# Optimization experiments

Hardware: AMD Instinct MI355X
Metric: run time of the kernel (lower is better)

## Reference

```python
import jax, jax.numpy as jnp
import numpy as np

P_DROP = 0.6  # F.dropout default training=True in the original forward

def setup_inputs() -> dict:
    key = jax.random.key(0)
    k1, k2, k3, k4 = jax.random.split(key, 4)
    B, T, V, F, K, O = 32, 12, 1000, 64, 3, 64
    x = jax.random.normal(k1, (B, T, V, F), dtype=jnp.float32)
    Att = jax.random.uniform(k2, (V, V), dtype=jnp.float32)
    cheb = jax.random.normal(k3, (K, V, V), dtype=jnp.float32)   # Chebyshev polynomials T_k(L)
    Theta = jax.random.normal(k4, (K, F, O), dtype=jnp.float32)  # per-order feature transforms
    return {"x": x, "Att": Att, "cheb": cheb, "Theta": Theta}

def reference(x, Att, cheb, Theta):
    # x: [B,T,V,F]; Att: [V,V]; cheb: [K,V,V]; Theta: [K,F,O]
    B, T, V, F = x.shape
    K = cheb.shape[0]
    keep = 1.0 - P_DROP
    # Original draws a fresh dropout mask per (time_step, k); replicate with a fixed key.
    mask = jax.random.bernoulli(jax.random.key(42), keep, (T, K, V, V))
    TkA = cheb * Att                                   # [K,V,V] attention-weighted polynomial
    M = jnp.where(mask, TkA[None] / keep, 0.0)         # [T,K,V,V] inverted dropout
    # rhs = T_k_with_at @ graph_signal, batched over (b,t,k)
    rhs = jnp.einsum('tkuv,btvf->btkuf', M, x)         # [B,T,K,V,F]
    # sum_k rhs_k @ Theta_k  -> [B,T,V,O]; matches permute(0,3,1,2) of stacked outputs
    out = jnp.einsum('btkuf,kfo->btuo', rhs, Theta)
    return jax.nn.relu(out)
```

## Files before the change

kernel.cpp:

```cpp
#include <hip/hip_runtime.h>
#include <hip/hip_bf16.h>
#include <stdint.h>


typedef __attribute__((ext_vector_type(8))) short short8;
typedef __attribute__((ext_vector_type(4))) float f32x4;

__device__ __forceinline__ ushort f2bf(float f) {
  __hip_bfloat16 h = __float2bfloat16(f);
  return *reinterpret_cast<ushort*>(&h);
}

__device__ __forceinline__ void threefry2x32(uint32_t c0, uint32_t c1,
                                             uint32_t& o0, uint32_t& o1) {
  const uint32_t ks0 = 0u;
  const uint32_t ks1 = 42u;
  const uint32_t ks2 = ks0 ^ ks1 ^ 0x1BD11BDAu;
  uint32_t x0 = c0 + ks0;
  uint32_t x1 = c1 + ks1;
#define TFR(r) { x0 += x1; x1 = (x1 << (r)) | (x1 >> (32 - (r))); x1 ^= x0; }
  TFR(13) TFR(15) TFR(26) TFR(6)
  x0 += ks1; x1 += ks2 + 1u;
  TFR(17) TFR(29) TFR(16) TFR(24)
  x0 += ks2; x1 += ks0 + 2u;
  TFR(13) TFR(15) TFR(26) TFR(6)
  x0 += ks0; x1 += ks1 + 3u;
  TFR(17) TFR(29) TFR(16) TFR(24)
  x0 += ks1; x1 += ks2 + 4u;
  TFR(13) TFR(15) TFR(26) TFR(6)
  x0 += ks2; x1 += ks0 + 5u;
#undef TFR
  o0 = x0; o1 = x1;
}

__global__ void build_m(const float* __restrict__ Att,
                        const float* __restrict__ cheb,
                        ushort* __restrict__ Mf) {
  const uint32_t idx = blockIdx.x * 256u + threadIdx.x;
  const uint32_t j = idx & 7u;
  const uint32_t lane = (idx >> 3) & 63u;
  const uint32_t ks = (idx >> 9) & 1u;
  const uint32_t c = (idx >> 10) & 15u;
  const uint32_t u16 = (idx >> 14) & 63u;
  const uint32_t tk = idx >> 20;
  const uint32_t up = u16 * 16u + (lane & 15u);
  const uint32_t vp = c * 64u + ks * 32u + (lane >> 4) * 8u + j;
  float val = 0.f;
  if ((vp < 1000u) & (up < 1000u)) {
    const uint32_t flat = (tk * 1000u + up) * 1000u + vp;
    uint32_t o0, o1;
    threefry2x32(0u, flat, o0, o1);
    const uint32_t bits = o0 ^ o1;
    const float u = __uint_as_float((bits >> 9) | 0x3f800000u) - 1.0f;
    if (u < 0.4f) {
      val = cheb[(tk % 3u) * 1000000u + up * 1000u + vp] *
            Att[up * 1000u + vp] * 2.5f;
    }
  }
  Mf[idx] = f2bf(val);
}

__global__ void transpose_x(const float* __restrict__ x,
                            ushort* __restrict__ xt) {
  __shared__ float lt[64][65];
  const int vc = blockIdx.x, t = blockIdx.y, b = blockIdx.z;
  const int tid = threadIdx.x;
  const int v0 = vc * 64;
#pragma unroll
  for (int i = 0; i < 4; ++i) {
    const int c = i * 256 + tid;
    const int vi = c >> 4, f4 = c & 15;
    float4 q = make_float4(0.f, 0.f, 0.f, 0.f);
    if (v0 + vi < 1000)
      q = *(const float4*)(x + ((((size_t)b * 12 + t) * 1000 + v0 + vi) << 6) + f4 * 4);
    lt[f4 * 4 + 0][vi] = q.x;
    lt[f4 * 4 + 1][vi] = q.y;
    lt[f4 * 4 + 2][vi] = q.z;
    lt[f4 * 4 + 3][vi] = q.w;
  }
  __syncthreads();
  const int f = tid >> 2, g = tid & 3;
  alignas(16) ushort tmp[16];
#pragma unroll
  for (int j = 0; j < 16; ++j) tmp[j] = f2bf(lt[f][g * 16 + j]);
  const size_t base = ((size_t)(t * 2048 + b * 64 + f)) << 10;
  *(uint4*)(xt + base + v0 + g * 16)     = *(const uint4*)&tmp[0];
  *(uint4*)(xt + base + v0 + g * 16 + 8) = *(const uint4*)&tmp[8];
}

#define LDT 72

#define MFMA(a, b, c) __builtin_amdgcn_mfma_f32_16x16x32_bf16((a), (b), (c), 0, 0, 0)

#define BURST(BP)                                                             \
  do {                                                                        \
    const ushort* sBc = (BP);                                                 \
    _Pragma("unroll")                                                         \
    for (int ks = 0; ks < 2; ++ks) {                                          \
      short8 bv[4];                                                           \
      _Pragma("unroll")                                                       \
      for (int ni = 0; ni < 4; ++ni) {                                        \
        const int row = wn * 64 + ni * 16 + l15;                              \
        bv[ni] = *(const short8*)&sBc[row * 64 + (((ks * 4 + quad) ^ rsw) * 8)]; \
      }                                                                       \
      _Pragma("unroll")                                                       \
      for (int k = 0; k < 3; ++k)                                             \
        _Pragma("unroll")                                                     \
        for (int mi = 0; mi < 2; ++mi)                                        \
          _Pragma("unroll")                                                   \
          for (int ni = 0; ni < 4; ++ni)                                      \
            pacc[k][mi][ni] = MFMA(afr[k][mi][ks], bv[ni], pacc[k][mi][ni]);  \
    }                                                                         \
  } while (0)

#define LOAD_A(VC)                                                            \
  do {                                                                        \
    _Pragma("unroll")                                                         \
    for (int k = 0; k < 3; ++k)                                               \
      _Pragma("unroll")                                                       \
      for (int mi = 0; mi < 2; ++mi)                                          \
        _Pragma("unroll")                                                     \
        for (int ks = 0; ks < 2; ++ks)                                        \
          afr[k][mi][ks] = *(const short8*)(Mf + fb[k][mi] +                  \
                             (size_t)(VC) * 1024 + ks * 512 + lane * 8);      \
  } while (0)

#define SOFT_BARRIER()                                                        \
  do {                                                                        \
    asm volatile("s_waitcnt lgkmcnt(0)" ::: "memory");                        \
    __builtin_amdgcn_s_barrier();                                             \
    __builtin_amdgcn_sched_barrier(0);                                        \
  } while (0)

__global__ __launch_bounds__(512, 1)
void cheb_main(const ushort* __restrict__ Mf, const ushort* __restrict__ xt,
               const float* __restrict__ Theta, float* __restrict__ out) {
  __shared__ __align__(16) ushort smem[23040];
  const int tid = threadIdx.x;
  const int lane = tid & 63;
  const int w = tid >> 6;
  const int wu = w >> 1, wn = w & 1;
  const int quad = lane >> 4, l15 = lane & 15;
  const int bid = blockIdx.x;
  const int nt = (bid >> 3) & 15;
  const int ut = bid & 7;
  const int t  = bid >> 7;
  const int u0 = ut * 128, n0 = nt * 128;

  ushort* buf0 = smem;
  ushort* buf1 = smem + 8192;
  ushort* sP  = smem + w * (32 * LDT);
  ushort* sTh = smem + 18432;

  const int srow = lane >> 3;
  const int gchunk = (lane & 7) ^ srow;
  const int rsw = l15 & 7;

  const size_t xrow0 = (size_t)(t * 2048 + n0);
  const int rr0 = 8 * (w * 2 + 0) + srow;
  const int rr1 = 8 * (w * 2 + 1) + srow;
  const size_t gx0 = ((xrow0 + rr0) << 10) + gchunk * 8;
  const size_t gx1 = ((xrow0 + rr1) << 10) + gchunk * 8;
  const int da0 = (w * 2 + 0) * 512 + lane * 8;
  const int da1 = (w * 2 + 1) * 512 + lane * 8;

  size_t fb[3][2];
#pragma unroll
  for (int k = 0; k < 3; ++k)
#pragma unroll
    for (int mi = 0; mi < 2; ++mi)
      fb[k][mi] = ((size_t)((t * 3 + k) * 64 + ut * 8 + wu * 2 + mi)) << 14;

  f32x4 pacc[3][2][4];
#pragma unroll
  for (int k = 0; k < 3; ++k)
#pragma unroll
    for (int i = 0; i < 2; ++i)
#pragma unroll
      for (int j = 0; j < 4; ++j) pacc[k][i][j] = f32x4{0.f, 0.f, 0.f, 0.f};

  short8 afr[3][2][2];
  uint4 p0, p1;

  p0 = *(const uint4*)(xt + gx0);
  p1 = *(const uint4*)(xt + gx1);
  *(uint4*)&buf0[da0] = p0;
  *(uint4*)&buf0[da1] = p1;
  __syncthreads();

#pragma unroll 1
  for (int it = 0; it < 8; ++it) {
    const int vc = it * 2;
    LOAD_A(vc);
    p0 = *(const uint4*)(xt + gx0 + (size_t)(vc + 1) * 64);
    p1 = *(const uint4*)(xt + gx1 + (size_t)(vc + 1) * 64);
    __builtin_amdgcn_s_setprio(1);
    BURST(buf0);
    __builtin_amdgcn_s_setprio(0);
    *(uint4*)&buf1[da0] = p0;
    *(uint4*)&buf1[da1] = p1;
    SOFT_BARRIER();
    LOAD_A(vc + 1);
    if (vc + 1 < 15) {
      p0 = *(const uint4*)(xt + gx0 + (size_t)(vc + 2) * 64);
      p1 = *(const uint4*)(xt + gx1 + (size_t)(vc + 2) * 64);
    }
    __builtin_amdgcn_s_setprio(1);
    BURST(buf1);
    __builtin_amdgcn_s_setprio(0);
    if (vc + 1 < 15) {
      *(uint4*)&buf0[da0] = p0;
      *(uint4*)&buf0[da1] = p1;
    }
    SOFT_BARRIER();
  }

  f32x4 oacc[2][4];
#pragma unroll
  for (int i = 0; i < 2; ++i)
#pragma unroll
    for (int j = 0; j < 4; ++j) oacc[i][j] = f32x4{0.f, 0.f, 0.f, 0.f};

#pragma unroll
  for (int k = 0; k < 3; ++k) {
    __syncthreads();
#pragma unroll
    for (int mi = 0; mi < 2; ++mi)
#pragma unroll
      for (int ni = 0; ni < 4; ++ni)
#pragma unroll
        for (int r = 0; r < 4; ++r)
          sP[(mi * 16 + quad * 4 + r) * LDT + ni * 16 + l15] = f2bf(pacc[k][mi][ni][r]);
    for (int e = tid; e < 4096; e += 512) {
      const int f = e >> 6, o = e & 63;
      sTh[o * LDT + f] = f2bf(Theta[k * 4096 + e]);
    }
    __syncthreads();
#pragma unroll
    for (int ks = 0; ks < 2; ++ks) {
      short8 a2[2], b2[4];
#pragma unroll
      for (int mi = 0; mi < 2; ++mi)
        a2[mi] = *(const short8*)&sP[(mi * 16 + l15) * LDT + ks * 32 + quad * 8];
#pragma unroll
      for (int ni = 0; ni < 4; ++ni)
        b2[ni] = *(const short8*)&sTh[(ni * 16 + l15) * LDT + ks * 32 + quad * 8];
#pragma unroll
      for (int mi = 0; mi < 2; ++mi)
#pragma unroll
        for (int ni = 0; ni < 4; ++ni)
          oacc[mi][ni] = MFMA(a2[mi], b2[ni], oacc[mi][ni]);
    }
  }

#pragma unroll
  for (int mi = 0; mi < 2; ++mi) {
    const int u_base = u0 + wu * 32 + mi * 16 + quad * 4;
#pragma unroll
    for (int ni = 0; ni < 4; ++ni) {
      const int n = n0 + wn * 64 + ni * 16 + l15;
      const int b = n >> 6, oo = n & 63;
      float* op = out + (((size_t)b * 12 + t) * 1000) * 64 + oo;
#pragma unroll
      for (int r = 0; r < 4; ++r) {
        const int u = u_base + r;
        if (u < 1000) op[(size_t)u * 64] = fmaxf(oacc[mi][ni][r], 0.f);
      }
    }
  }
}

extern "C" void kernel_launch(void* const* d_in, const int* in_sizes, int n_in,
                              void* d_out, int out_size, void* d_ws, size_t ws_size,
                              hipStream_t stream) {
  const float* x     = (const float*)d_in[0];
  const float* Att   = (const float*)d_in[1];
  const float* cheb  = (const float*)d_in[2];
  const float* Theta = (const float*)d_in[3];
  float* out = (float*)d_out;

  ushort* Mf  = (ushort*)d_ws;
  ushort* xtw = Mf + 37748736ull;

  build_m<<<147456, 256, 0, stream>>>(Att, cheb, Mf);
  transpose_x<<<dim3(16, 12, 32), 256, 0, stream>>>(x, xtw);
  cheb_main<<<1536, 512, 0, stream>>>(Mf, xtw, Theta, out);
}
```

Before: 306.1 us.

## Reassociate Theta projection before graph GEMM and fuse K into reduction

```diff
diff --git a/kernel.cpp b/kernel.cpp
--- a/kernel.cpp
+++ b/kernel.cpp
@@ -9,6 +9,15 @@
 __device__ __forceinline__ ushort f2bf(float f) {
   __hip_bfloat16 h = __float2bfloat16(f);
   return *reinterpret_cast<ushort*>(&h);
+}
+
+__device__ __forceinline__ short8 cvt8(float4 a, float4 b) {
+  short8 r;
+  r[0] = (short)f2bf(a.x); r[1] = (short)f2bf(a.y);
+  r[2] = (short)f2bf(a.z); r[3] = (short)f2bf(a.w);
+  r[4] = (short)f2bf(b.x); r[5] = (short)f2bf(b.y);
+  r[6] = (short)f2bf(b.z); r[7] = (short)f2bf(b.w);
+  return r;
 }
 
 __device__ __forceinline__ void threefry2x32(uint32_t c0, uint32_t c1,
@@ -60,214 +69,199 @@
   Mf[idx] = f2bf(val);
 }
 
-__global__ void transpose_x(const float* __restrict__ x,
-                            ushort* __restrict__ xt) {
-  __shared__ float lt[64][65];
-  const int vc = blockIdx.x, t = blockIdx.y, b = blockIdx.z;
-  const int tid = threadIdx.x;
+#define MFMA(a, b, c) __builtin_amdgcn_mfma_f32_16x16x32_bf16((a), (b), (c), 0, 0, 0)
+
+__global__ __launch_bounds__(192, 1)
+void build_yt(const float* __restrict__ x, const float* __restrict__ Theta,
+              ushort* __restrict__ yt, int NR, int bq0) {
+  __shared__ __align__(16) ushort sm[13824];
+  const int tid = threadIdx.x, lane = tid & 63, w = tid >> 6;
+  const int quad = lane >> 4, l15 = lane & 15;
+  const int vc = blockIdx.x, t = blockIdx.y, bb = blockIdx.z;
+  const int b = bq0 + bb;
   const int v0 = vc * 64;
-#pragma unroll
-  for (int i = 0; i < 4; ++i) {
-    const int c = i * 256 + tid;
-    const int vi = c >> 4, f4 = c & 15;
-    float4 q = make_float4(0.f, 0.f, 0.f, 0.f);
-    if (v0 + vi < 1000)
-      q = *(const float4*)(x + ((((size_t)b * 12 + t) * 1000 + v0 + vi) << 6) + f4 * 4);
-    lt[f4 * 4 + 0][vi] = q.x;
-    lt[f4 * 4 + 1][vi] = q.y;
-    lt[f4 * 4 + 2][vi] = q.z;
-    lt[f4 * 4 + 3][vi] = q.w;
+
+  for (int e = tid; e < 12288; e += 192) {
+    const int k = e >> 12, rem = e & 4095, f = rem >> 6, o = rem & 63;
+    sm[k * 4608 + o * 72 + f] = f2bf(Theta[e]);
   }
   __syncthreads();
-  const int f = tid >> 2, g = tid & 3;
-  alignas(16) ushort tmp[16];
-#pragma unroll
-  for (int j = 0; j < 16; ++j) tmp[j] = f2bf(lt[f][g * 16 + j]);
-  const size_t base = ((size_t)(t * 2048 + b * 64 + f)) << 10;
-  *(uint4*)(xt + base + v0 + g * 16)     = *(const uint4*)&tmp[0];
-  *(uint4*)(xt + base + v0 + g * 16 + 8) = *(const uint4*)&tmp[8];
-}
-
-#define LDT 72
-
-#define MFMA(a, b, c) __builtin_amdgcn_mfma_f32_16x16x32_bf16((a), (b), (c), 0, 0, 0)
-
-#define BURST(BP)                                                             \
-  do {                                                                        \
-    const ushort* sBc = (BP);                                                 \
+
+  f32x4 pacc[4][4];
+#pragma unroll
+  for (int i = 0; i < 4; ++i)
+#pragma unroll
+    for (int j = 0; j < 4; ++j) pacc[i][j] = f32x4{0.f, 0.f, 0.f, 0.f};
+
+  const ushort* sTh = sm + w * 4608;
+  const float* xb = x + (((size_t)b * 12 + t) * 1000) * 64;
+
+#pragma unroll
+  for (int ks = 0; ks < 2; ++ks) {
+    short8 av[4], bv[4];
+#pragma unroll
+    for (int mi = 0; mi < 4; ++mi)
+      av[mi] = *(const short8*)&sTh[(mi * 16 + l15) * 72 + ks * 32 + quad * 8];
+#pragma unroll
+    for (int ni = 0; ni < 4; ++ni) {
+      const int v = v0 + ni * 16 + l15;
+      float4 c0 = make_float4(0.f, 0.f, 0.f, 0.f);
+      float4 c1 = make_float4(0.f, 0.f, 0.f, 0.f);
+      if (v < 1000) {
+        const float* row = xb + (size_t)v * 64 + ks * 32 + quad * 8;
+        c0 = *(const float4*)row;
+        c1 = *(const float4*)(row + 4);
+      }
+      bv[ni] = cvt8(c0, c1);
+    }
+#pragma unroll
+    for (int mi = 0; mi < 4; ++mi)
+#pragma unroll
+      for (int ni = 0; ni < 4; ++ni)
+        pacc[mi][ni] = MFMA(av[mi], bv[ni], pacc[mi][ni]);
+  }
+
+  ushort* sY = sm + w * 4608;
+#pragma unroll
+  for (int mi = 0; mi < 4; ++mi)
+#pragma unroll
+    for (int ni = 0; ni < 4; ++ni)
+#pragma unroll
+      for (int r = 0; r < 4; ++r)
+        sY[(mi * 16 + quad * 4 + r) * 72 + ni * 16 + l15] = f2bf(pacc[mi][ni][r]);
+
+  const int seg = lane & 7;
+#pragma unroll
+  for (int p = 0; p < 8; ++p) {
+    const int o = p * 8 + (lane >> 3);
+    const uint4 val = *(const uint4*)&sY[o * 72 + seg * 8];
+    *(uint4*)(yt + (((size_t)(w * 12 + t) * (size_t)NR + (size_t)bb * 64 + o) << 10)
+                 + v0 + seg * 8) = val;
+  }
+}
+
+#define LOAD_A(AR, C)                                                         \
+  do {                                                                        \
+    const size_t base_ = ((tk3 + (size_t)((C) >> 4)) << 20) +                 \
+                         ((size_t)((C) & 15) << 10) + lane * 8;               \
+    _Pragma("unroll")                                                         \
+    for (int mi = 0; mi < 4; ++mi)                                            \
+      _Pragma("unroll")                                                       \
+      for (int ks = 0; ks < 2; ++ks)                                          \
+        AR[mi][ks] = *(const short8*)(Mf + base_ +                            \
+                       ((size_t)(u16b + mi) << 14) + (ks << 9));              \
+  } while (0)
+
+#define LOAD_B(P0, P1, P2, P3, C)                                             \
+  do {                                                                        \
+    const size_t yb_ = (((size_t)(((C) >> 4) * 12 + t) * (size_t)NR + n0 +    \
+                         brow) << 10) + ((size_t)((C) & 15) << 6) + gch * 8;  \
+    P0 = *(const uint4*)(yt + yb_);                                           \
+    P1 = *(const uint4*)(yt + yb_ + (64 << 10));                              \
+    P2 = *(const uint4*)(yt + yb_ + (128 << 10));                             \
+    P3 = *(const uint4*)(yt + yb_ + (192 << 10));                             \
+  } while (0)
+
+#define WRITE_B(P0, P1, P2, P3, BUF)                                          \
+  do {                                                                        \
+    *(uint4*)&(BUF)[tid * 8]          = P0;                                   \
+    *(uint4*)&(BUF)[4096 + tid * 8]   = P1;                                   \
+    *(uint4*)&(BUF)[8192 + tid * 8]   = P2;                                   \
+    *(uint4*)&(BUF)[12288 + tid * 8]  = P3;                                   \
+  } while (0)
+
+#define BURST(BUF, AR)                                                        \
+  do {                                                                        \
     _Pragma("unroll")                                                         \
     for (int ks = 0; ks < 2; ++ks) {                                          \
       short8 bv[4];                                                           \
       _Pragma("unroll")                                                       \
       for (int ni = 0; ni < 4; ++ni) {                                        \
-        const int row = wn * 64 + ni * 16 + l15;                              \
-        bv[ni] = *(const short8*)&sBc[row * 64 + (((ks * 4 + quad) ^ rsw) * 8)]; \
+        const int row_ = wc * 64 + ni * 16 + l15;                             \
+        bv[ni] = *(const short8*)&(BUF)[row_ * 64 +                           \
+                                        ((((ks * 4 + quad) ^ rsw)) << 3)];    \
       }                                                                       \
       _Pragma("unroll")                                                       \
-      for (int k = 0; k < 3; ++k)                                             \
+      for (int mi = 0; mi < 4; ++mi)                                          \
         _Pragma("unroll")                                                     \
-        for (int mi = 0; mi < 2; ++mi)                                        \
-          _Pragma("unroll")                                                   \
-          for (int ni = 0; ni < 4; ++ni)                                      \
-            pacc[k][mi][ni] = MFMA(afr[k][mi][ks], bv[ni], pacc[k][mi][ni]);  \
+        for (int ni = 0; ni < 4; ++ni)                                        \
+          pacc[mi][ni] = MFMA(AR[mi][ks], bv[ni], pacc[mi][ni]);              \
     }                                                                         \
   } while (0)
 
-#define LOAD_A(VC)                                                            \
-  do {                                                                        \
-    _Pragma("unroll")                                                         \
-    for (int k = 0; k < 3; ++k)                                               \
-      _Pragma("unroll")                                                       \
-      for (int mi = 0; mi < 2; ++mi)                                          \
-        _Pragma("unroll")                                                     \
-        for (int ks = 0; ks < 2; ++ks)                                        \
-          afr[k][mi][ks] = *(const short8*)(Mf + fb[k][mi] +                  \
-                             (size_t)(VC) * 1024 + ks * 512 + lane * 8);      \
-  } while (0)
-
-#define SOFT_BARRIER()                                                        \
-  do {                                                                        \
-    asm volatile("s_waitcnt lgkmcnt(0)" ::: "memory");                        \
-    __builtin_amdgcn_s_barrier();                                             \
-    __builtin_amdgcn_sched_barrier(0);                                        \
-  } while (0)
-
-__global__ __launch_bounds__(512, 1)
-void cheb_main(const ushort* __restrict__ Mf, const ushort* __restrict__ xt,
-               const float* __restrict__ Theta, float* __restrict__ out) {
-  __shared__ __align__(16) ushort smem[23040];
-  const int tid = threadIdx.x;
-  const int lane = tid & 63;
-  const int w = tid >> 6;
-  const int wu = w >> 1, wn = w & 1;
-  const int quad = lane >> 4, l15 = lane & 15;
-  const int bid = blockIdx.x;
-  const int nt = (bid >> 3) & 15;
-  const int ut = bid & 7;
-  const int t  = bid >> 7;
-  const int u0 = ut * 128, n0 = nt * 128;
+__global__ __launch_bounds__(512, 2)
+void gemm_main(const ushort* __restrict__ Mf, const ushort* __restrict__ yt,
+               float* __restrict__ out, int NR, int bq0, int nblocks) {
+  __shared__ __align__(16) ushort smem[32768];
+  const int tid = threadIdx.x, lane = tid & 63, w = tid >> 6;
+  const int wr = w >> 2, wc = w & 3;
+  const int quad = lane >> 4, l15 = lane & 15, rsw = l15 & 7;
+  const int q = nblocks >> 3;
+  const int swz = ((int)blockIdx.x & 7) * q + ((int)blockIdx.x >> 3);
+  const int ntcnt = NR >> 8;
+  const int ntile = swz % ntcnt;
+  const int rem = swz / ntcnt;
+  const int ut = rem & 7, t = rem >> 3;
+  const int u0 = ut * 128, n0 = ntile * 256;
 
   ushort* buf0 = smem;
-  ushort* buf1 = smem + 8192;
-  ushort* sP  = smem + w * (32 * LDT);
-  ushort* sTh = smem + 18432;
-
-  const int srow = lane >> 3;
-  const int gchunk = (lane & 7) ^ srow;
-  const int rsw = l15 & 7;
-
-  const size_t xrow0 = (size_t)(t * 2048 + n0);
-  const int rr0 = 8 * (w * 2 + 0) + srow;
-  const int rr1 = 8 * (w * 2 + 1) + srow;
-  const size_t gx0 = ((xrow0 + rr0) << 10) + gchunk * 8;
-  const size_t gx1 = ((xrow0 + rr1) << 10) + gchunk * 8;
-  const int da0 = (w * 2 + 0) * 512 + lane * 8;
-  const int da1 = (w * 2 + 1) * 512 + lane * 8;
-
-  size_t fb[3][2];
-#pragma unroll
-  for (int k = 0; k < 3; ++k)
-#pragma unroll
-    for (int mi = 0; mi < 2; ++mi)
-      fb[k][mi] = ((size_t)((t * 3 + k) * 64 + ut * 8 + wu * 2 + mi)) << 14;
-
-  f32x4 pacc[3][2][4];
-#pragma unroll
-  for (int k = 0; k < 3; ++k)
-#pragma unroll
-    for (int i = 0; i < 2; ++i)
-#pragma unroll
-      for (int j = 0; j < 4; ++j) pacc[k][i][j] = f32x4{0.f, 0.f, 0.f, 0.f};
-
-  short8 afr[3][2][2];
-  uint4 p0, p1;
-
-  p0 = *(const uint4*)(xt + gx0);
-  p1 = *(const uint4*)(xt + gx1);
-  *(uint4*)&buf0[da0] = p0;
-  *(uint4*)&buf0[da1] = p1;
+  ushort* buf1 = smem + 16384;
+
+  const int gch = (tid & 7) ^ ((tid >> 3) & 7);
+  const int brow = tid >> 3;
+  const int u16b = ut * 8 + wr * 4;
+  const size_t tk3 = (size_t)(t * 3);
+
+  f32x4 pacc[4][4];
+#pragma unroll
+  for (int i = 0; i < 4; ++i)
+#pragma unroll
+    for (int j = 0; j < 4; ++j) pacc[i][j] = f32x4{0.f, 0.f, 0.f, 0.f};
+
+  short8 aA[4][2], aB[4][2];
+  uint4 p0, p1, p2, p3, q0, q1, q2, q3;
+
+  LOAD_B(p0, p1, p2, p3, 0);
+  WRITE_B(p0, p1, p2, p3, buf0);
+  LOAD_A(aA, 0);
   __syncthreads();
 
 #pragma unroll 1
-  for (int it = 0; it < 8; ++it) {
-    const int vc = it * 2;
-    LOAD_A(vc);
-    p0 = *(const uint4*)(xt + gx0 + (size_t)(vc + 1) * 64);
-    p1 = *(const uint4*)(xt + gx1 + (size_t)(vc + 1) * 64);
+  for (int it = 0; it < 24; ++it) {
+    const int c1 = it * 2 + 1;
+    LOAD_A(aB, it * 2 + 1);
+    LOAD_B(q0, q1, q2, q3, it * 2 + 1);
     __builtin_amdgcn_s_setprio(1);
-    BURST(buf0);
+    BURST(buf0, aA);
     __builtin_amdgcn_s_setprio(0);
-    *(uint4*)&buf1[da0] = p0;
-    *(uint4*)&buf1[da1] = p1;
-    SOFT_BARRIER();
-    LOAD_A(vc + 1);
-    if (vc + 1 < 15) {
-      p0 = *(const uint4*)(xt + gx0 + (size_t)(vc + 2) * 64);
-      p1 = *(const uint4*)(xt + gx1 + (size_t)(vc + 2) * 64);
+    WRITE_B(q0, q1, q2, q3, buf1);
+    __syncthreads();
+    if (c1 < 47) {
+      LOAD_A(aA, c1 + 1);
+      LOAD_B(p0, p1, p2, p3, c1 + 1);
     }
     __builtin_amdgcn_s_setprio(1);
-    BURST(buf1);
+    BURST(buf1, aB);
     __builtin_amdgcn_s_setprio(0);
-    if (vc + 1 < 15) {
-      *(uint4*)&buf0[da0] = p0;
-      *(uint4*)&buf0[da1] = p1;
-    }
-    SOFT_BARRIER();
-  }
-
-  f32x4 oacc[2][4];
-#pragma unroll
-  for (int i = 0; i < 2; ++i)
-#pragma unroll
-    for (int j = 0; j < 4; ++j) oacc[i][j] = f32x4{0.f, 0.f, 0.f, 0.f};
-
-#pragma unroll
-  for (int k = 0; k < 3; ++k) {
+    if (c1 < 47) WRITE_B(p0, p1, p2, p3, buf0);
     __syncthreads();
-#pragma unroll
-    for (int mi = 0; mi < 2; ++mi)
-#pragma unroll
-      for (int ni = 0; ni < 4; ++ni)
-#pragma unroll
-        for (int r = 0; r < 4; ++r)
-          sP[(mi * 16 + quad * 4 + r) * LDT + ni * 16 + l15] = f2bf(pacc[k][mi][ni][r]);
-    for (int e = tid; e < 4096; e += 512) {
-      const int f = e >> 6, o = e & 63;
-      sTh[o * LDT + f] = f2bf(Theta[k * 4096 + e]);
-    }
-    __syncthreads();
-#pragma unroll
-    for (int ks = 0; ks < 2; ++ks) {
-      short8 a2[2], b2[4];
-#pragma unroll
-      for (int mi = 0; mi < 2; ++mi)
-        a2[mi] = *(const short8*)&sP[(mi * 16 + l15) * LDT + ks * 32 + quad * 8];
-#pragma unroll
-      for (int ni = 0; ni < 4; ++ni)
-        b2[ni] = *(const short8*)&sTh[(ni * 16 + l15) * LDT + ks * 32 + quad * 8];
-#pragma unroll
-      for (int mi = 0; mi < 2; ++mi)
-#pragma unroll
-        for (int ni = 0; ni < 4; ++ni)
-          oacc[mi][ni] = MFMA(a2[mi], b2[ni], oacc[mi][ni]);
-    }
-  }
-
-#pragma unroll
-  for (int mi = 0; mi < 2; ++mi) {
-    const int u_base = u0 + wu * 32 + mi * 16 + quad * 4;
+  }
+
+  const int ubase = u0 + wr * 64;
+  const int nbase = n0 + wc * 64;
+#pragma unroll
+  for (int mi = 0; mi < 4; ++mi)
 #pragma unroll
     for (int ni = 0; ni < 4; ++ni) {
-      const int n = n0 + wn * 64 + ni * 16 + l15;
-      const int b = n >> 6, oo = n & 63;
-      float* op = out + (((size_t)b * 12 + t) * 1000) * 64 + oo;
+      const int n = nbase + ni * 16 + l15;
+      const int b = bq0 + (n >> 6), o = n & 63;
+      float* op = out + (((size_t)b * 12 + t) * 1000) * 64 + o;
 #pragma unroll
       for (int r = 0; r < 4; ++r) {
-        const int u = u_base + r;
-        if (u < 1000) op[(size_t)u * 64] = fmaxf(oacc[mi][ni][r], 0.f);
+        const int u = ubase + mi * 16 + quad * 4 + r;
+        if (u < 1000) op[(size_t)u * 64] = fmaxf(pacc[mi][ni][r], 0.f);
       }
     }
-  }
 }
 
 extern "C" void kernel_launch(void* const* d_in, const int* in_sizes, int n_in,
@@ -279,10 +273,18 @@
   const float* Theta = (const float*)d_in[3];
   float* out = (float*)d_out;
 
-  ushort* Mf  = (ushort*)d_ws;
-  ushort* xtw = Mf + 37748736ull;
+  ushort* Mf = (ushort*)d_ws;
+  ushort* yt = Mf + 37748736ull;
 
   build_m<<<147456, 256, 0, stream>>>(Att, cheb, Mf);
-  transpose_x<<<dim3(16, 12, 32), 256, 0, stream>>>(x, xtw);
-  cheb_main<<<1536, 512, 0, stream>>>(Mf, xtw, Theta, out);
-}
+
+  if (ws_size >= 226492416ull) {
+    build_yt<<<dim3(16, 12, 32), 192, 0, stream>>>(x, Theta, yt, 2048, 0);
+    gemm_main<<<768, 512, 0, stream>>>(Mf, yt, out, 2048, 0, 768);
+  } else {
+    for (int qq = 0; qq < 4; ++qq) {
+      build_yt<<<dim3(16, 12, 8), 192, 0, stream>>>(x, Theta, yt, 512, qq * 8);
+      gemm_main<<<192, 512, 0, stream>>>(Mf, yt, out, 512, qq * 8, 192);
+    }
+  }
+}
```

After: 392.8 us. +28.3%, slower.
